# Performance work log

Hardware: AMD Instinct MI355X
Metric: run time of the kernel (lower is better)

The kernel has to match this reference:

```python
import jax, jax.numpy as jnp
import numpy as np

D_MODEL = 512

def setup_inputs() -> dict:
    key = jax.random.key(0)
    kx, kw, kb = jax.random.split(key, 3)
    x = jax.random.normal(kx, (4, 4096, D_MODEL), dtype=jnp.float32)
    # node_proj Linear(d_model, d_model): weight [D, D], bias [D]
    lim = 1.0 / np.sqrt(D_MODEL)
    W_node = jax.random.uniform(kw, (D_MODEL, D_MODEL), minval=-lim, maxval=lim, dtype=jnp.float32)
    b_node = jax.random.uniform(kb, (D_MODEL,), minval=-lim, maxval=lim, dtype=jnp.float32)
    return {"x": x, "W_node": W_node, "b_node": b_node}

def reference(x, W_node, b_node):
    # node_features = relu(x @ W^T + b)   [B, S, D]
    node = jax.nn.relu(jnp.einsum('bsd,ed->bse', x, W_node) + b_node)
    # unscaled self-attention: softmax(node @ node^T) @ node
    scores = jnp.einsum('bsd,btd->bst', node, node)  # [B, S, S]
    attn = jax.nn.softmax(scores, axis=-1)
    out = jnp.einsum('bst,btd->bsd', attn, node)
    # dropout is identity in eval mode
    return out
```

## Files before the change

### kernel.cpp

```cpp
#include <hip/hip_runtime.h>

#define D_MODEL 512
#define SEQ     4096
#define BATCH   4
#define M_TOT   (BATCH*SEQ)
#define NT      (SEQ/32)
#define WS_NEEDED ((size_t)2 * M_TOT * D_MODEL * 2)

typedef float  f32x4  __attribute__((ext_vector_type(4)));
typedef __bf16 bf16x8 __attribute__((ext_vector_type(8)));

#define LGKM_BARRIER() asm volatile("s_waitcnt lgkmcnt(0)\n\ts_barrier" ::: "memory")

union FU { float f; unsigned int u; };
__device__ __forceinline__ unsigned short f_to_bf16(float f) {
    FU c; c.f = f;
    unsigned int r = c.u + 0x7fffu + ((c.u >> 16) & 1u);
    return (unsigned short)(r >> 16);
}

__device__ __forceinline__ void split_pack(float f0, float f1,
        unsigned int& hp, unsigned int& lp) {
    FU u0, u1; u0.f = f0; u1.f = f1;
    unsigned int h0 = u0.u & 0xFFFF0000u, h1 = u1.u & 0xFFFF0000u;
    hp = (h0 >> 16) | h1;
    FU t0, t1; t0.u = h0; t1.u = h1;
    float l0 = f0 - t0.f, l1 = f1 - t1.f;
    lp = (unsigned)f_to_bf16(l0) | ((unsigned)f_to_bf16(l1) << 16);
}

template<int CTRL>
__device__ __forceinline__ float dpp_mov(float x) {
    union { float f; int i; } u, r;
    u.f = x;
    r.i = __builtin_amdgcn_update_dpp(u.i, u.i, CTRL, 0xF, 0xF, false);
    return r.f;
}
__device__ __forceinline__ float red_max16(float x) {
    x = fmaxf(x, dpp_mov<0xB1>(x));
    x = fmaxf(x, dpp_mov<0x4E>(x));
    x = fmaxf(x, dpp_mov<0x141>(x));
    x = fmaxf(x, dpp_mov<0x140>(x));
    return x;
}
__device__ __forceinline__ float red_sum16(float x) {
    x += dpp_mov<0xB1>(x);
    x += dpp_mov<0x4E>(x);
    x += dpp_mov<0x141>(x);
    x += dpp_mov<0x140>(x);
    return x;
}

extern "C" __global__ __launch_bounds__(256, 2) void proj_kernel(
        const float* __restrict__ x, const float* __restrict__ w,
        const float* __restrict__ bias,
        unsigned short* __restrict__ node_bf, unsigned short* __restrict__ nodeT_bf) {
    __shared__ unsigned short Ah[128][40], Al[128][40], Bh[128][40], Bl[128][40];
    const int tid  = threadIdx.x;
    const int lane = tid & 63;
    const int wv   = tid >> 6;
    const int lr   = lane & 15;
    const int quad = lane >> 4;
    const int row0 = blockIdx.x * 128;
    const int col0 = blockIdx.y * 128;
    const int wm   = (wv & 1) * 64;
    const int wn   = (wv >> 1) * 64;

    f32x4 acc[4][4];
    #pragma unroll
    for (int i = 0; i < 4; ++i)
        #pragma unroll
        for (int j = 0; j < 4; ++j) acc[i][j] = (f32x4){0.f,0.f,0.f,0.f};

    for (int kc = 0; kc < D_MODEL; kc += 32) {
        #pragma unroll
        for (int i = 0; i < 2; ++i) {
            int idx = i*256 + tid;
            int r = idx >> 2, c8 = (idx & 3) * 8;
            const float* xp = x + (size_t)(row0 + r)*D_MODEL + kc + c8;
            const float* wp = w + (size_t)(col0 + r)*D_MODEL + kc + c8;
            float4 a0 = *(const float4*)(xp);
            float4 a1 = *(const float4*)(xp + 4);
            float4 b0 = *(const float4*)(wp);
            float4 b1 = *(const float4*)(wp + 4);
            uint4 hA, lA, hB, lB;
            split_pack(a0.x, a0.y, hA.x, lA.x);
            split_pack(a0.z, a0.w, hA.y, lA.y);
            split_pack(a1.x, a1.y, hA.z, lA.z);
            split_pack(a1.z, a1.w, hA.w, lA.w);
            split_pack(b0.x, b0.y, hB.x, lB.x);
            split_pack(b0.z, b0.w, hB.y, lB.y);
            split_pack(b1.x, b1.y, hB.z, lB.z);
            split_pack(b1.z, b1.w, hB.w, lB.w);
            *(uint4*)&Ah[r][c8] = hA;
            *(uint4*)&Al[r][c8] = lA;
            *(uint4*)&Bh[r][c8] = hB;
            *(uint4*)&Bl[r][c8] = lB;
        }
        __syncthreads();

        bf16x8 ah[4], al[4], bh[4], bl[4];
        #pragma unroll
        for (int i = 0; i < 4; ++i) {
            ah[i] = *(const bf16x8*)&Ah[wm + i*16 + lr][quad*8];
            al[i] = *(const bf16x8*)&Al[wm + i*16 + lr][quad*8];
            bh[i] = *(const bf16x8*)&Bh[wn + i*16 + lr][quad*8];
            bl[i] = *(const bf16x8*)&Bl[wn + i*16 + lr][quad*8];
        }
        #pragma unroll
        for (int i = 0; i < 4; ++i)
            #pragma unroll
            for (int j = 0; j < 4; ++j) {
                acc[i][j] = __builtin_amdgcn_mfma_f32_16x16x32_bf16(al[i], bh[j], acc[i][j], 0, 0, 0);
                acc[i][j] = __builtin_amdgcn_mfma_f32_16x16x32_bf16(ah[i], bl[j], acc[i][j], 0, 0, 0);
                acc[i][j] = __builtin_amdgcn_mfma_f32_16x16x32_bf16(ah[i], bh[j], acc[i][j], 0, 0, 0);
            }
        __syncthreads();
    }

    #pragma unroll
    for (int j = 0; j < 4; ++j) {
        int col = col0 + wn + j*16 + lr;
        float bv = bias[col];
        #pragma unroll
        for (int i = 0; i < 4; ++i) {
            #pragma unroll
            for (int r = 0; r < 4; ++r) {
                float v = acc[i][j][r] + bv;
                v = v > 0.0f ? v : 0.0f;
                unsigned short us = f_to_bf16(v);
                int row = row0 + wm + i*16 + quad*4 + r;
                node_bf[(size_t)row*D_MODEL + col] = us;
                int b = row >> 12, si = row & 4095;
                nodeT_bf[((size_t)(b*D_MODEL + col))*SEQ + si] = us;
            }
        }
    }
}

extern "C" __global__ __launch_bounds__(512, 2) void flash_kernel(
        const unsigned short* __restrict__ node,
        const unsigned short* __restrict__ nodeT,
        float* __restrict__ out) {
    __shared__ unsigned short Ks[2][32][512];
    __shared__ unsigned short Vt[512][32];
    __shared__ unsigned short Ps[4][16][40];
    __shared__ float          Sm[4][2][16];
    __shared__ int            Lf[8];
    const int tid  = threadIdx.x;
    const int lane = tid & 63;
    const int wv   = tid >> 6;
    const int qg   = wv & 3;
    const int kh   = wv >> 2;
    const int lr   = lane & 15;
    const int quad = lane >> 4;
    const int bb   = blockIdx.y;
    const int q0   = blockIdx.x * 64;
    const int ktd  = blockIdx.x * 2;

    const unsigned short* nb  = node  + (size_t)bb * SEQ * D_MODEL;
    const unsigned short* ntb = nodeT + (size_t)bb * D_MODEL * SEQ;

    bf16x8 qf[16];
    const int qrow = q0 + qg*16 + lr;
    #pragma unroll
    for (int t = 0; t < 16; ++t)
        qf[t] = *reinterpret_cast<const bf16x8*>(&nb[(size_t)qrow*D_MODEL + t*32 + quad*8]);

    f32x4 o[16];
    #pragma unroll
    for (int n = 0; n < 16; ++n) o[n] = (f32x4){0.f,0.f,0.f,0.f};
    float m_run[4] = {-3.0e38f,-3.0e38f,-3.0e38f,-3.0e38f};
    float l_run[4] = {0.f,0.f,0.f,0.f};

    auto ktOf = [&](int i) { return i < 2 ? ktd + i : i - 2; };

    auto stageK = [&](int kt, int buf) {
        #pragma unroll
        for (int i = 0; i < 4; ++i) {
            int r = wv*4 + i;
            const unsigned short* g = nb + (size_t)(kt*32 + r)*D_MODEL + ((lane ^ (r & 7)) << 3);
            __builtin_amdgcn_global_load_lds(
                (const __attribute__((address_space(1))) unsigned int*)g,
                (__attribute__((address_space(3))) unsigned int*)&Ks[buf][r][0],
                16, 0, 0);
        }
    };
    auto stageV = [&](int kt) {
        #pragma unroll
        for (int i = 0; i < 4; ++i) {
            int d0 = (wv*4 + i) * 16;
            int d  = d0 + (lane >> 2);
            const unsigned short* g = ntb + (size_t)d*SEQ + kt*32 + ((((lane & 3) ^ (d & 3))) << 3);
            __builtin_amdgcn_global_load_lds(
                (const __attribute__((address_space(1))) unsigned int*)g,
                (__attribute__((address_space(3))) unsigned int*)&Vt[d0][0],
                16, 0, 0);
        }
    };

    stageK(ktOf(0), 0);
    __syncthreads();

    const int kxor = lr & 7;
    const int vxor = lr & 3;

    for (int idx = 0; idx < NT + 2; ++idx) {
        const int cur = idx & 1;
        const int kt  = ktOf(idx);
        const bool force = (idx >= 2) && ((kt >> 1) == blockIdx.x);
        if (idx + 1 < NT + 2) stageK(ktOf(idx + 1), cur ^ 1);

        f32x4 sacc = (f32x4){0.f,0.f,0.f,0.f};
        __builtin_amdgcn_s_setprio(1);
        #pragma unroll
        for (int t = 0; t < 16; ++t) {
            bf16x8 kb = *reinterpret_cast<const bf16x8*>(
                &Ks[cur][kh*16 + lr][(((t<<2)|quad) ^ kxor) << 3]);
            sacc = __builtin_amdgcn_mfma_f32_16x16x32_bf16(qf[t], kb, sacc, 0, 0, 0);
        }
        __builtin_amdgcn_s_setprio(0);

        float mx[4];
        #pragma unroll
        for (int r = 0; r < 4; ++r) mx[r] = red_max16(sacc[r]);
        if (lr == 0) {
            #pragma unroll
            for (int r = 0; r < 4; ++r) Sm[qg][kh][quad*4 + r] = mx[r];
        }
        LGKM_BARRIER();

        float jm[4];
        bool live = false;
        #pragma unroll
        for (int r = 0; r < 4; ++r) {
            jm[r] = fmaxf(mx[r], Sm[qg][kh ^ 1][quad*4 + r]);
            live = live || (jm[r] > m_run[r] - 25.0f);
        }
        const bool skip = force || !__any(live);

        if (!skip) {
            float alpha[4];
            #pragma unroll
            for (int r = 0; r < 4; ++r) {
                float mnew = fmaxf(m_run[r], jm[r]);
                alpha[r]   = __expf(m_run[r] - mnew);
                float p    = __expf(sacc[r] - mnew);
                m_run[r]   = mnew;
                Ps[qg][quad*4 + r][kh*16 + lr] = f_to_bf16(p);
                float rs   = red_sum16(p);
                l_run[r] = l_run[r]*alpha[r] + rs;
            }
            bool need = !(alpha[0]==1.f && alpha[1]==1.f && alpha[2]==1.f && alpha[3]==1.f);
            if (__any(need)) {
                #pragma unroll
                for (int n = 0; n < 16; ++n) {
                    #pragma unroll
                    for (int r = 0; r < 4; ++r) o[n][r] *= alpha[r];
                }
            }
        }
        if (lane == 0) Lf[wv] = skip ? 0 : 1;
        LGKM_BARRIER();

        const bool block_live = (Lf[0]|Lf[1]|Lf[2]|Lf[3]|Lf[4]|Lf[5]|Lf[6]|Lf[7]) != 0;
        if (block_live) {
            stageV(kt);
            __syncthreads();
            if (!skip) {
                bf16x8 pa = *reinterpret_cast<const bf16x8*>(&Ps[qg][lr][quad*8]);
                __builtin_amdgcn_s_setprio(1);
                #pragma unroll
                for (int n = 0; n < 16; ++n) {
                    int dblk = kh*16 + n;
                    bf16x8 vb = *reinterpret_cast<const bf16x8*>(
                        &Vt[dblk*16 + lr][(quad ^ vxor) << 3]);
                    o[n] = __builtin_amdgcn_mfma_f32_16x16x32_bf16(pa, vb, o[n], 0, 0, 0);
                }
                __builtin_amdgcn_s_setprio(0);
            }
        }

        __syncthreads();
    }

    if (lr == 0) {
        #pragma unroll
        for (int r = 0; r < 4; ++r) Sm[qg][kh][quad*4 + r] = l_run[r];
    }
    __syncthreads();
    #pragma unroll
    for (int r = 0; r < 4; ++r) {
        float l_tot = l_run[r] + Sm[qg][kh ^ 1][quad*4 + r];
        float inv   = 1.0f / l_tot;
        int row = q0 + qg*16 + quad*4 + r;
        float* obase = out + ((size_t)bb * SEQ + row) * D_MODEL;
        #pragma unroll
        for (int n = 0; n < 16; ++n)
            obase[(kh*16 + n)*16 + lr] = o[n][r] * inv;
    }
}

extern "C" void kernel_launch(void* const* d_in, const int* in_sizes, int n_in,
                              void* d_out, int out_size, void* d_ws, size_t ws_size,
                              hipStream_t stream) {
    const float* x = (const float*)d_in[0];
    const float* w = (const float*)d_in[1];
    const float* b = (const float*)d_in[2];
    float* out = (float*)d_out;
    unsigned short* node_bf  = (unsigned short*)d_ws;
    unsigned short* nodeT_bf = node_bf + (size_t)M_TOT * D_MODEL;
    const size_t out_bytes = (size_t)out_size * 4;

    (void)hipMemsetAsync(d_out, 0x42, out_bytes, stream);

    if (d_ws == 0 || ws_size < WS_NEEDED) {
        (void)hipMemsetAsync(d_out, 0x4F, out_bytes, stream);
        return;
    }

    (void)hipGetLastError();
    proj_kernel<<<dim3(M_TOT/128, D_MODEL/128), dim3(256), 0, stream>>>(x, w, b, node_bf, nodeT_bf);
    hipError_t ep = hipGetLastError();
    flash_kernel<<<dim3(SEQ/64, BATCH), dim3(512), 0, stream>>>(node_bf, nodeT_bf, out);
    hipError_t ef = hipGetLastError();

    if (ep != hipSuccess) {
        (void)hipMemsetAsync(d_out, 0x49, out_bytes, stream);
    } else if (ef != hipSuccess) {
        (void)hipMemsetAsync(d_out, 0x4B, out_bytes, stream);
    }
}
```

Baseline: 359.6 us.

## Load projection operands directly into registers with double-buffered prefetch, dropping LDS

```diff
diff --git a/kernel.cpp b/kernel.cpp
--- a/kernel.cpp
+++ b/kernel.cpp
@@ -55,7 +55,6 @@
         const float* __restrict__ x, const float* __restrict__ w,
         const float* __restrict__ bias,
         unsigned short* __restrict__ node_bf, unsigned short* __restrict__ nodeT_bf) {
-    __shared__ unsigned short Ah[128][40], Al[128][40], Bh[128][40], Bl[128][40];
     const int tid  = threadIdx.x;
     const int lane = tid & 63;
     const int wv   = tid >> 6;
@@ -66,47 +65,43 @@
     const int wm   = (wv & 1) * 64;
     const int wn   = (wv >> 1) * 64;
 
+    const float* xb = x + (size_t)(row0 + wm + lr)*D_MODEL + quad*8;
+    const float* wb = w + (size_t)(col0 + wn + lr)*D_MODEL + quad*8;
+
     f32x4 acc[4][4];
     #pragma unroll
     for (int i = 0; i < 4; ++i)
         #pragma unroll
         for (int j = 0; j < 4; ++j) acc[i][j] = (f32x4){0.f,0.f,0.f,0.f};
 
-    for (int kc = 0; kc < D_MODEL; kc += 32) {
-        #pragma unroll
-        for (int i = 0; i < 2; ++i) {
-            int idx = i*256 + tid;
-            int r = idx >> 2, c8 = (idx & 3) * 8;
-            const float* xp = x + (size_t)(row0 + r)*D_MODEL + kc + c8;
-            const float* wp = w + (size_t)(col0 + r)*D_MODEL + kc + c8;
-            float4 a0 = *(const float4*)(xp);
-            float4 a1 = *(const float4*)(xp + 4);
-            float4 b0 = *(const float4*)(wp);
-            float4 b1 = *(const float4*)(wp + 4);
-            uint4 hA, lA, hB, lB;
-            split_pack(a0.x, a0.y, hA.x, lA.x);
-            split_pack(a0.z, a0.w, hA.y, lA.y);
-            split_pack(a1.x, a1.y, hA.z, lA.z);
-            split_pack(a1.z, a1.w, hA.w, lA.w);
-            split_pack(b0.x, b0.y, hB.x, lB.x);
-            split_pack(b0.z, b0.w, hB.y, lB.y);
-            split_pack(b1.x, b1.y, hB.z, lB.z);
-            split_pack(b1.z, b1.w, hB.w, lB.w);
-            *(uint4*)&Ah[r][c8] = hA;
-            *(uint4*)&Al[r][c8] = lA;
-            *(uint4*)&Bh[r][c8] = hB;
-            *(uint4*)&Bl[r][c8] = lB;
-        }
-        __syncthreads();
-
-        bf16x8 ah[4], al[4], bh[4], bl[4];
+    auto load_split = [&](int kc, bf16x8 ah[4], bf16x8 al[4],
+                                  bf16x8 bh[4], bf16x8 bl[4]) {
         #pragma unroll
         for (int i = 0; i < 4; ++i) {
-            ah[i] = *(const bf16x8*)&Ah[wm + i*16 + lr][quad*8];
-            al[i] = *(const bf16x8*)&Al[wm + i*16 + lr][quad*8];
-            bh[i] = *(const bf16x8*)&Bh[wn + i*16 + lr][quad*8];
-            bl[i] = *(const bf16x8*)&Bl[wn + i*16 + lr][quad*8];
-        }
+            const float* p = xb + (size_t)i*16*D_MODEL + kc;
+            float4 r0 = *(const float4*)(p);
+            float4 r1 = *(const float4*)(p + 4);
+            uint4 h, l;
+            split_pack(r0.x, r0.y, h.x, l.x);
+            split_pack(r0.z, r0.w, h.y, l.y);
+            split_pack(r1.x, r1.y, h.z, l.z);
+            split_pack(r1.z, r1.w, h.w, l.w);
+            ah[i] = *(bf16x8*)&h;  al[i] = *(bf16x8*)&l;
+        }
+        #pragma unroll
+        for (int j = 0; j < 4; ++j) {
+            const float* p = wb + (size_t)j*16*D_MODEL + kc;
+            float4 r0 = *(const float4*)(p);
+            float4 r1 = *(const float4*)(p + 4);
+            uint4 h, l;
+            split_pack(r0.x, r0.y, h.x, l.x);
+            split_pack(r0.z, r0.w, h.y, l.y);
+            split_pack(r1.x, r1.y, h.z, l.z);
+            split_pack(r1.z, r1.w, h.w, l.w);
+            bh[j] = *(bf16x8*)&h;  bl[j] = *(bf16x8*)&l;
+        }
+    };
+    auto mfma_all = [&](bf16x8 ah[4], bf16x8 al[4], bf16x8 bh[4], bf16x8 bl[4]) {
         #pragma unroll
         for (int i = 0; i < 4; ++i)
             #pragma unroll
@@ -115,7 +110,16 @@
                 acc[i][j] = __builtin_amdgcn_mfma_f32_16x16x32_bf16(ah[i], bl[j], acc[i][j], 0, 0, 0);
                 acc[i][j] = __builtin_amdgcn_mfma_f32_16x16x32_bf16(ah[i], bh[j], acc[i][j], 0, 0, 0);
             }
-        __syncthreads();
+    };
+
+    bf16x8 ahA[4], alA[4], bhA[4], blA[4];
+    bf16x8 ahB[4], alB[4], bhB[4], blB[4];
+    load_split(0, ahA, alA, bhA, blA);
+    for (int kc = 0; kc < D_MODEL; kc += 64) {
+        load_split(kc + 32, ahB, alB, bhB, blB);
+        mfma_all(ahA, alA, bhA, blA);
+        if (kc + 64 < D_MODEL) load_split(kc + 64, ahA, alA, bhA, blA);
+        mfma_all(ahB, alB, bhB, blB);
     }
 
     #pragma unroll
```

New measurement: 385.1 us. 7.1% more time.
